# Performance work log

Measured on AMD Instinct MI355X. Metric: run time of the kernel, lower is better.

## Reference

```python
import jax, jax.numpy as jnp
import numpy as np

B, R, N, DN, DR, H, Q, NB = 32, 10, 512, 128, 128, 128, 256, 16


def setup_inputs() -> dict:
    key = jax.random.key(0)
    ks = jax.random.split(key, 14)
    inp = {
        'node_features': jax.random.normal(ks[0], (B, N, DN), jnp.float32),
        'relation_features': jax.random.normal(ks[1], (B, R, DR), jnp.float32),
        'adj': jax.random.uniform(ks[2], (B, R, N, N), jnp.float32),
        'obs': jax.random.normal(ks[3], (B, Q, H), jnp.float32),
        'node_mask': jnp.ones((B, N), jnp.float32),
        'obs_mask': jnp.ones((B, Q), jnp.float32),
        # RGCN params (single layer: hidden_dims=[128])
        'Wb': jax.random.normal(ks[4], (NB, (DN + DR) * R), jnp.float32) * 0.02,  # bottleneck (no bias)
        'Ww': jax.random.normal(ks[5], (H, NB), jnp.float32) * 0.1,               # weight (no bias)
        'rgcn_bias': jnp.zeros((), jnp.float32),                                   # scalar bias (filled 0)
        # ContextQueryAttention params
        'w_C': jax.random.normal(ks[6], (H,), jnp.float32) * 0.05,
        'w_Q': jax.random.normal(ks[7], (H,), jnp.float32) * 0.05,
        'w_CQ': jax.random.normal(ks[8], (H,), jnp.float32) * 0.05,
        'cq_bias': jnp.zeros((), jnp.float32),
        # ReprAggregator output linear (shared for both directions)
        'lin_W': jax.random.normal(ks[9], (H, 4 * H), jnp.float32) * 0.02,
        'lin_b': jnp.zeros((H,), jnp.float32),
    }
    return inp


def _masked_softmax(s, mask, axis):
    return jax.nn.softmax(jnp.where(mask > 0, s, -jnp.inf), axis=axis)


def _rgcn(node_features, relation_features, adj, Wb, Ww, rgcn_bias):
    b, n = node_features.shape[0], node_features.shape[1]
    # per-relation concat: (B,R,N,DN+DR)
    nf = jnp.broadcast_to(node_features[:, None], (b, R, n, node_features.shape[-1]))
    rf = jnp.broadcast_to(relation_features[:, :, None, :], (b, R, n, relation_features.shape[-1]))
    cat = jnp.concatenate([nf, rf], axis=-1)
    # per-relation bmm, gathered in relation order along feature dim: (B,N,R*(DN+DR))
    sup = jnp.einsum('brnm,brmd->bnrd', adj, cat)
    sup = sup.reshape(b, n, R * cat.shape[-1])
    h = sup @ Wb.T            # (B,N,NB)
    h = h @ Ww.T              # (B,N,H)
    return jax.nn.sigmoid(h + rgcn_bias)


def _cqattn(ctx, query, ctx_mask, query_mask, w_C, w_Q, w_CQ, cq_bias):
    # trilinear similarity: (B,Lc,Lq)
    res_C = ctx @ w_C                                  # (B,Lc)
    res_Q = query @ w_Q                                # (B,Lq)
    res_CQ = jnp.einsum('bch,bqh->bcq', ctx * w_CQ, query)
    S = res_C[:, :, None] + res_Q[:, None, :] + res_CQ + cq_bias
    s_ctx = _masked_softmax(S, ctx_mask[:, :, None], axis=1)     # softmax over ctx dim
    s_query = _masked_softmax(S, query_mask[:, None, :], axis=2)  # softmax over query dim
    P = jnp.einsum('bcq,bqh->bch', s_query, query)
    Qm = jnp.einsum('bcq,bdq,bdh->bch', s_query, s_ctx, ctx)
    return jnp.concatenate([ctx, P, ctx * P, ctx * Qm], axis=-1)  # (B,Lc,4H)


def reference(node_features, relation_features, adj, obs, node_mask, obs_mask,
              Wb, Ww, rgcn_bias, w_C, w_Q, w_CQ, cq_bias, lin_W, lin_b):
    # GraphEncoder (single RGCN layer)
    node_repr = _rgcn(node_features, relation_features, adj, Wb, Ww, rgcn_bias)
    # ReprAggregator between obs text repr and node repr
    a1 = _cqattn(obs, node_repr, obs_mask, node_mask, w_C, w_Q, w_CQ, cq_bias)
    a2 = _cqattn(node_repr, obs, node_mask, obs_mask, w_C, w_Q, w_CQ, cq_bias)
    h_og = a1 @ lin_W.T + lin_b   # (B,Q,H)
    h_go = a2 @ lin_W.T + lin_b   # (B,N,H)
    return h_og, h_go
```

## Files before the change

### kernel.cpp

```cpp
#include <hip/hip_runtime.h>
#include <hip/hip_bf16.h>
#include <stdint.h>

typedef unsigned short u16;
typedef __attribute__((ext_vector_type(8))) short short8;
typedef __attribute__((ext_vector_type(4))) float f32x4;

#define DEVI static __device__ __forceinline__

constexpr int B = 32, R = 10, N = 512, H = 128, Q = 256, NB = 16;
constexpr int KWB = 2560;

DEVI u16 f2u(float f) { return __builtin_bit_cast(unsigned short, __float2bfloat16(f)); }
DEVI float u2f(u16 u) { union { uint32_t i; float f; } c; c.i = ((uint32_t)u) << 16; return c.f; }

DEVI float wredmax(float v) { for (int o = 32; o; o >>= 1) v = fmaxf(v, __shfl_xor(v, o)); return v; }
DEVI float wredsum(float v) { for (int o = 32; o; o >>= 1) v += __shfl_xor(v, o); return v; }

__global__ __launch_bounds__(256) void k_prep(
    const float* __restrict__ linW, u16* __restrict__ linWb,
    const float* __restrict__ Wb, u16* __restrict__ WbB,
    const float* __restrict__ Ww, u16* __restrict__ WwB,
    const float* __restrict__ rf, float* __restrict__ vv,
    const float* __restrict__ obs, const float* __restrict__ wC,
    const float* __restrict__ wQ, const float* __restrict__ wCQ,
    u16* __restrict__ obsW, float* __restrict__ a_o, float* __restrict__ d_o) {
  int bid = blockIdx.x, t = threadIdx.x;
  if (bid < 64) {
    int i = bid * 256 + t;
    float4 f = ((const float4*)linW)[i];
    ushort4 o;
    o.x = f2u(f.x); o.y = f2u(f.y); o.z = f2u(f.z); o.w = f2u(f.w);
    ((ushort4*)linWb)[i] = o;
  } else if (bid < 144) {
    int rk = (bid - 64) * 2 + (t >> 7);
    int d = t & 127;
    int r = rk / NB, k = rk % NB;
    WbB[(long)rk * 128 + d] = f2u(Wb[(long)k * KWB + r * 256 + d]);
  } else if (bid < 160) {
    int idx = (bid - 144) * 256 + t;
    int h = idx >> 5, kb = idx & 31;
    WwB[idx] = (kb < NB) ? f2u(Ww[h * NB + kb]) : (u16)0;
  } else if (bid < 1440) {
    int w = t >> 6, lane = t & 63;
    int gid = (bid - 160) * 4 + w;
    int b = gid / (R * NB), rk = gid % (R * NB), r = rk / NB, k = rk % NB;
    float s = 0.f;
    for (int dd = 0; dd < 2; ++dd) {
      int d = lane + dd * 64;
      s += rf[((long)b * R + r) * H + d] * Wb[(long)k * KWB + r * 256 + 128 + d];
    }
    s = wredsum(s);
    if (lane == 0) vv[((long)b * R + r) * NB + k] = s;
  } else {
    int row = (bid - 1440) * 2 + (t >> 7);
    int tt = t & 127;
    float x = obs[(long)row * H + tt];
    obsW[(long)row * H + tt] = f2u(x * wCQ[tt]);
    float aa = wredsum(x * wC[tt]);
    float dd2 = wredsum(x * wQ[tt]);
    __shared__ float sa[4], sd[4];
    int wv = t >> 6;
    if ((t & 63) == 0) { sa[wv] = aa; sd[wv] = dd2; }
    __syncthreads();
    if ((t & 127) == 0) {
      int h = t >> 7;
      a_o[row] = sa[h * 2] + sa[h * 2 + 1];
      d_o[row] = sd[h * 2] + sd[h * 2 + 1];
    }
  }
}

template <bool INF32>
__global__ void k_transpose(const void* __restrict__ in, u16* __restrict__ out, int Rr, int Cc) {
  __shared__ u16 tile[32][33];
  int batch = blockIdx.z;
  int c0 = blockIdx.x * 32, r0 = blockIdx.y * 32;
  int tx = threadIdx.x, ty = threadIdx.y;
  for (int i = 0; i < 4; i++) {
    int r = r0 + ty + i * 8, c = c0 + tx;
    if (INF32) tile[ty + i * 8][tx] = f2u(((const float*)in)[((long)batch * Rr + r) * Cc + c]);
    else       tile[ty + i * 8][tx] = ((const u16*)in)[((long)batch * Rr + r) * Cc + c];
  }
  __syncthreads();
  for (int i = 0; i < 4; i++) {
    int c = c0 + ty + i * 8, r = r0 + tx;
    out[((long)batch * Cc + c) * Rr + r] = tile[tx][ty + i * 8];
  }
}

template <bool AF32, bool BF32, int CMODE, bool TRANSC, int BMODE, bool RGRID, int UNROLL>
__global__ __launch_bounds__(64) void gemm_bt(const void* __restrict__ Av, const void* __restrict__ Btv,
                                              void* __restrict__ Cp, float* __restrict__ C2,
                                              const float* __restrict__ bias,
                                              int Mdim, int Ndim, int Kdim,
                                              long sA, long sBt, long sC, long sC2) {
  int batch = blockIdx.y;
  int ab = batch, bb = batch;
  if (RGRID) { ab = batch % R; bb = batch / R; }
  int ntn = Ndim >> 4;
  int mt = blockIdx.x / ntn, nt = blockIdx.x % ntn;
  int lane = threadIdx.x;
  int rw = lane & 15, kq = lane >> 4;
  long aoff = (long)ab * sA + (long)(mt * 16 + rw) * Kdim + kq * 8;
  long boff = (long)bb * sBt + (long)(nt * 16 + rw) * Kdim + kq * 8;
  f32x4 acc = {0.f, 0.f, 0.f, 0.f};
#pragma unroll UNROLL
  for (int k = 0; k < Kdim; k += 32) {
    short8 av, bv;
    if (AF32) {
      const float* ap = (const float*)Av + aoff + k;
      float4 f0 = *(const float4*)(ap);
      float4 f1 = *(const float4*)(ap + 4);
      av[0] = (short)f2u(f0.x); av[1] = (short)f2u(f0.y);
      av[2] = (short)f2u(f0.z); av[3] = (short)f2u(f0.w);
      av[4] = (short)f2u(f1.x); av[5] = (short)f2u(f1.y);
      av[6] = (short)f2u(f1.z); av[7] = (short)f2u(f1.w);
    } else {
      av = *(const short8*)((const u16*)Av + aoff + k);
    }
    if (BF32) {
      const float* bp = (const float*)Btv + boff + k;
      float4 f0 = *(const float4*)(bp);
      float4 f1 = *(const float4*)(bp + 4);
      bv[0] = (short)f2u(f0.x); bv[1] = (short)f2u(f0.y);
      bv[2] = (short)f2u(f0.z); bv[3] = (short)f2u(f0.w);
      bv[4] = (short)f2u(f1.x); bv[5] = (short)f2u(f1.y);
      bv[6] = (short)f2u(f1.z); bv[7] = (short)f2u(f1.w);
    } else {
      bv = *(const short8*)((const u16*)Btv + boff + k);
    }
    acc = __builtin_amdgcn_mfma_f32_16x16x32_bf16(av, bv, acc, 0, 0, 0);
  }
  int gc = nt * 16 + rw;
  float cb = (BMODE == 1) ? bias[gc] : 0.f;
  for (int i = 0; i < 4; i++) {
    int gr = mt * 16 + (kq * 4 + i);
    float val = acc[i] + cb;
    if (BMODE == 2) val += bias[(long)batch * NB + gr];
    if (CMODE == 2) {
      ((float*)Cp)[(long)batch * sC + (long)gr * Ndim + gc] = val;
      C2[(long)batch * sC2 + (long)gc * Mdim + gr] = val;
    } else {
      long idx = TRANSC ? ((long)gc * Mdim + gr) : ((long)gr * Ndim + gc);
      if (CMODE == 1) ((float*)Cp)[(long)batch * sC + idx] = val;
      else            ((u16*)Cp)[(long)batch * sC + idx] = f2u(val);
    }
  }
}

__global__ __launch_bounds__(256) void k_rgcn(
    const float* __restrict__ adj, const u16* __restrict__ tT,
    const u16* __restrict__ WwB, const float* __restrict__ rb,
    const float* __restrict__ wC, const float* __restrict__ wQ,
    u16* __restrict__ nr, float* __restrict__ b_n, float* __restrict__ c_n) {
  int ntile = blockIdx.x, b = blockIdx.y;
  int n0 = ntile * 16;
  int tid = threadIdx.x;
  int w = tid >> 6, lane = tid & 63;
  int rw = lane & 15, kq = lane >> 4;
  __shared__ float hred[4][16][17];
  __shared__ __align__(16) u16 hbf[16][32];
  __shared__ float bpc[4][16][2];
  float rbv = rb[0];

  f32x4 acc = {0.f, 0.f, 0.f, 0.f};
#pragma unroll 4
  for (int j = 0; j < 40; ++j) {
    int kkk = w + 4 * j;
    int r = kkk >> 4, k = (kkk & 15) * 32;
    const float* ap = adj + (((long)(b * R + r) * N) + n0 + rw) * N + k + kq * 8;
    float4 f0 = *(const float4*)ap;
    float4 f1 = *(const float4*)(ap + 4);
    short8 av;
    av[0] = (short)f2u(f0.x); av[1] = (short)f2u(f0.y);
    av[2] = (short)f2u(f0.z); av[3] = (short)f2u(f0.w);
    av[4] = (short)f2u(f1.x); av[5] = (short)f2u(f1.y);
    av[6] = (short)f2u(f1.z); av[7] = (short)f2u(f1.w);
    short8 bv = *(const short8*)(tT + ((long)(b * R + r) * NB + rw) * N + k + kq * 8);
    acc = __builtin_amdgcn_mfma_f32_16x16x32_bf16(av, bv, acc, 0, 0, 0);
  }
  for (int i = 0; i < 4; i++) hred[w][kq * 4 + i][rw] = acc[i];
  __syncthreads();
  {
    int n = tid >> 4, kb = tid & 15;
    float s = hred[0][n][kb] + hred[1][n][kb] + hred[2][n][kb] + hred[3][n][kb];
    hbf[n][kb] = f2u(s);
    hbf[n][kb + 16] = 0;
  }
  __syncthreads();

  float bsum[4] = {0.f, 0.f, 0.f, 0.f}, csum[4] = {0.f, 0.f, 0.f, 0.f};
  for (int half = 0; half < 2; ++half) {
    int nt = w * 2 + half;
    short8 av = *(const short8*)&hbf[rw][kq * 8];
    short8 bv = *(const short8*)(WwB + (long)(nt * 16 + rw) * 32 + kq * 8);
    f32x4 a2 = {0.f, 0.f, 0.f, 0.f};
    a2 = __builtin_amdgcn_mfma_f32_16x16x32_bf16(av, bv, a2, 0, 0, 0);
    int h = nt * 16 + rw;
    float wq = wQ[h], wc = wC[h];
    for (int i = 0; i < 4; i++) {
      float s = 1.f / (1.f + expf(-(a2[i] + rbv)));
      int n = n0 + kq * 4 + i;
      nr[((long)b * N + n) * H + h] = f2u(s);
      bsum[i] += s * wq;
      csum[i] += s * wc;
    }
  }
  for (int i = 0; i < 4; i++) {
    for (int o = 8; o; o >>= 1) { bsum[i] += __shfl_xor(bsum[i], o); csum[i] += __shfl_xor(csum[i], o); }
  }
  if (rw == 0)
    for (int i = 0; i < 4; i++) { bpc[w][kq * 4 + i][0] = bsum[i]; bpc[w][kq * 4 + i][1] = csum[i]; }
  __syncthreads();
  if (tid < 32) {
    int ns = tid & 15, which = tid >> 4;
    float s = bpc[0][ns][which] + bpc[1][ns][which] + bpc[2][ns][which] + bpc[3][ns][which];
    (which ? c_n : b_n)[(long)b * N + n0 + ns] = s;
  }
}

struct GPar {
  const u16* A; const u16* Bt; u16* C;
  int Mdim; int Kdim; long sA, sBt, sC; int tc;
};
__global__ __launch_bounds__(64) void gemm_quad(GPar p0, GPar p1, GPar p2, GPar p3, int Ndim) {
  int z = blockIdx.z;
  GPar p = (z == 0) ? p0 : (z == 1) ? p1 : (z == 2) ? p2 : p3;
  int batch = blockIdx.y;
  int ntn = Ndim >> 4;
  int mt = blockIdx.x / ntn, nt = blockIdx.x % ntn;
  if (mt * 16 >= p.Mdim) return;
  int lane = threadIdx.x;
  int rw = lane & 15, kq = lane >> 4;
  const u16* ap = p.A + (long)batch * p.sA + (long)(mt * 16 + rw) * p.Kdim + kq * 8;
  const u16* bp = p.Bt + (long)batch * p.sBt + (long)(nt * 16 + rw) * p.Kdim + kq * 8;
  f32x4 acc = {0.f, 0.f, 0.f, 0.f};
#pragma unroll 2
  for (int k = 0; k < p.Kdim; k += 32) {
    short8 av = *(const short8*)(ap + k);
    short8 bv = *(const short8*)(bp + k);
    acc = __builtin_amdgcn_mfma_f32_16x16x32_bf16(av, bv, acc, 0, 0, 0);
  }
  int gc = nt * 16 + rw;
  for (int i = 0; i < 4; i++) {
    int gr = mt * 16 + (kq * 4 + i);
    long idx = p.tc ? ((long)gc * p.Mdim + gr) : ((long)gr * Ndim + gc);
    p.C[(long)batch * p.sC + idx] = f2u(acc[i]);
  }
}

template <bool XF32>
__global__ __launch_bounds__(64) void gemm_cat(const void* __restrict__ Xv, const u16* __restrict__ P,
                                               const u16* __restrict__ Qm, const u16* __restrict__ Wt,
                                               const float* __restrict__ bias, float* __restrict__ out,
                                               int Mdim) {
  int batch = blockIdx.y;
  int ntn = H >> 4;
  int mt = blockIdx.x / ntn, nt = blockIdx.x % ntn;
  int lane = threadIdx.x;
  int rw = lane & 15, kq = lane >> 4;
  long arow = (long)batch * Mdim + (mt * 16 + rw);
  const u16* bp = Wt + (long)(nt * 16 + rw) * (4 * H) + kq * 8;
  f32x4 acc = {0.f, 0.f, 0.f, 0.f};
  for (int k = 0; k < 4 * H; k += 32) {
    int sec = k >> 7;
    int off = (k & 127) + kq * 8;
    long rb2 = arow * H + off;
    short8 av;
    if (sec == 0) {
      if (XF32) {
        const float* xp = (const float*)Xv + rb2;
        float4 f0 = *(const float4*)(xp);
        float4 f1 = *(const float4*)(xp + 4);
        av[0] = (short)f2u(f0.x); av[1] = (short)f2u(f0.y);
        av[2] = (short)f2u(f0.z); av[3] = (short)f2u(f0.w);
        av[4] = (short)f2u(f1.x); av[5] = (short)f2u(f1.y);
        av[6] = (short)f2u(f1.z); av[7] = (short)f2u(f1.w);
      } else {
        av = *(const short8*)((const u16*)Xv + rb2);
      }
    } else if (sec == 1) {
      av = *(const short8*)(P + rb2);
    } else {
      float xf[8];
      if (XF32) {
        const float* xp = (const float*)Xv + rb2;
        float4 f0 = *(const float4*)(xp);
        float4 f1 = *(const float4*)(xp + 4);
        xf[0] = f0.x; xf[1] = f0.y; xf[2] = f0.z; xf[3] = f0.w;
        xf[4] = f1.x; xf[5] = f1.y; xf[6] = f1.z; xf[7] = f1.w;
      } else {
        short8 xv = *(const short8*)((const u16*)Xv + rb2);
        for (int i = 0; i < 8; i++) xf[i] = u2f((u16)xv[i]);
      }
      short8 pv = *(const short8*)((sec == 2 ? P : Qm) + rb2);
      for (int i = 0; i < 8; i++) av[i] = (short)f2u(xf[i] * u2f((u16)pv[i]));
    }
    short8 bv = *(const short8*)(bp + k);
    acc = __builtin_amdgcn_mfma_f32_16x16x32_bf16(av, bv, acc, 0, 0, 0);
  }
  int gc = nt * 16 + rw;
  float cb = bias[gc];
  for (int i = 0; i < 4; i++) {
    int gr = mt * 16 + (kq * 4 + i);
    out[((long)batch * Mdim + gr) * H + gc] = acc[i] + cb;
  }
}

__global__ __launch_bounds__(256) void k_soft_both(
    const float* __restrict__ Mm, const float* __restrict__ MmT,
    const float* __restrict__ b_n, const float* __restrict__ c_n,
    const float* __restrict__ a_o, const float* __restrict__ d_o,
    const float* __restrict__ nmask, const float* __restrict__ omask,
    u16* __restrict__ sq1, u16* __restrict__ sc2,
    u16* __restrict__ sc1T, u16* __restrict__ sq2) {
  int bid = blockIdx.x;
  __shared__ float s1a[4], s2a[4];
  if (bid < B * Q) {
    int b = bid / Q;
    int t = threadIdx.x;
    long ro = bid;
    float v1[2], v2[2];
    for (int i = 0; i < 2; i++) {
      int n = t + 256 * i;
      float mv = Mm[ro * N + n];
      bool on = nmask[(long)b * N + n] > 0.f;
      v1[i] = on ? b_n[(long)b * N + n] + mv : -1e30f;
      v2[i] = on ? c_n[(long)b * N + n] + mv : -1e30f;
    }
    float m1 = wredmax(fmaxf(v1[0], v1[1]));
    float m2 = wredmax(fmaxf(v2[0], v2[1]));
    int wv = t >> 6;
    if ((t & 63) == 0) { s1a[wv] = m1; s2a[wv] = m2; }
    __syncthreads();
    m1 = fmaxf(fmaxf(s1a[0], s1a[1]), fmaxf(s1a[2], s1a[3]));
    m2 = fmaxf(fmaxf(s2a[0], s2a[1]), fmaxf(s2a[2], s2a[3]));
    __syncthreads();
    float e1[2], e2[2];
    e1[0] = expf(v1[0] - m1); e1[1] = expf(v1[1] - m1);
    e2[0] = expf(v2[0] - m2); e2[1] = expf(v2[1] - m2);
    float s1 = wredsum(e1[0] + e1[1]);
    float s2 = wredsum(e2[0] + e2[1]);
    if ((t & 63) == 0) { s1a[wv] = s1; s2a[wv] = s2; }
    __syncthreads();
    float r1 = 1.f / (s1a[0] + s1a[1] + s1a[2] + s1a[3]);
    float r2 = 1.f / (s2a[0] + s2a[1] + s2a[2] + s2a[3]);
    for (int i = 0; i < 2; i++) {
      int n = t + 256 * i;
      sq1[ro * N + n] = f2u(e1[i] * r1);
      sc2[ro * N + n] = f2u(e2[i] * r2);
    }
  } else {
    int id = bid - B * Q;
    int b = id / N;
    int o = threadIdx.x;
    long rn = id;
    float mv = MmT[rn * Q + o];
    bool on = omask[(long)b * Q + o] > 0.f;
    float v1 = on ? a_o[(long)b * Q + o] + mv : -1e30f;
    float v2 = on ? d_o[(long)b * Q + o] + mv : -1e30f;
    float m1 = wredmax(v1), m2 = wredmax(v2);
    int wv = o >> 6;
    if ((o & 63) == 0) { s1a[wv] = m1; s2a[wv] = m2; }
    __syncthreads();
    m1 = fmaxf(fmaxf(s1a[0], s1a[1]), fmaxf(s1a[2], s1a[3]));
    m2 = fmaxf(fmaxf(s2a[0], s2a[1]), fmaxf(s2a[2], s2a[3]));
    __syncthreads();
    float e1 = expf(v1 - m1), e2 = expf(v2 - m2);
    float s1 = wredsum(e1), s2 = wredsum(e2);
    if ((o & 63) == 0) { s1a[wv] = s1; s2a[wv] = s2; }
    __syncthreads();
    float r1 = 1.f / (s1a[0] + s1a[1] + s1a[2] + s1a[3]);
    float r2 = 1.f / (s2a[0] + s2a[1] + s2a[2] + s2a[3]);
    sc1T[rn * Q + o] = f2u(e1 * r1);
    sq2[rn * Q + o] = f2u(e2 * r2);
  }
}

extern "C" void kernel_launch(void* const* d_in, const int* in_sizes, int n_in,
                              void* d_out, int out_size, void* d_ws, size_t ws_size,
                              hipStream_t stream) {
  const float* nf    = (const float*)d_in[0];
  const float* rf    = (const float*)d_in[1];
  const float* adj   = (const float*)d_in[2];
  const float* obs   = (const float*)d_in[3];
  const float* nmask = (const float*)d_in[4];
  const float* omask = (const float*)d_in[5];
  const float* Wb    = (const float*)d_in[6];
  const float* Ww    = (const float*)d_in[7];
  const float* rb    = (const float*)d_in[8];
  const float* wC    = (const float*)d_in[9];
  const float* wQ    = (const float*)d_in[10];
  const float* wCQ   = (const float*)d_in[11];
  const float* linW  = (const float*)d_in[13];
  const float* linb  = (const float*)d_in[14];
  float* outp = (float*)d_out;

  char* w = (char*)d_ws;
  auto alloc = [&](size_t bytes) { char* p = w; w += (bytes + 255) & ~(size_t)255; return p; };
  u16*   linWb = (u16*)  alloc((size_t)H * 4 * H * 2);
  u16*   WbB   = (u16*)  alloc((size_t)R * NB * 128 * 2);
  u16*   WwB   = (u16*)  alloc((size_t)H * 32 * 2);
  float* vv    = (float*)alloc((size_t)B * R * NB * 4);
  u16*   obsW  = (u16*)  alloc((size_t)B * Q * H * 2);
  u16*   obsT  = (u16*)  alloc((size_t)B * H * Q * 2);
  float* a_o   = (float*)alloc((size_t)B * Q * 4);
  float* d_o   = (float*)alloc((size_t)B * Q * 4);
  float* b_n   = (float*)alloc((size_t)B * N * 4);
  float* c_n   = (float*)alloc((size_t)B * N * 4);
  u16*   nr    = (u16*)  alloc((size_t)B * N * H * 2);
  u16*   nrT   = (u16*)  alloc((size_t)B * H * N * 2);
  u16*   tT    = (u16*)  alloc((size_t)B * R * NB * N * 2);
  float* Mm    = (float*)alloc((size_t)B * Q * N * 4);
  float* MmT   = (float*)alloc((size_t)B * N * Q * 4);
  u16*   sq1   = (u16*)  alloc((size_t)B * Q * N * 2);
  u16*   sc2   = (u16*)  alloc((size_t)B * Q * N * 2);
  u16*   sc1T  = (u16*)  alloc((size_t)B * N * Q * 2);
  u16*   sq2   = (u16*)  alloc((size_t)B * N * Q * 2);
  u16*   P1    = (u16*)  alloc((size_t)B * Q * H * 2);
  u16*   T1T   = (u16*)  alloc((size_t)B * H * N * 2);
  u16*   Qm1   = (u16*)  alloc((size_t)B * Q * H * 2);
  u16*   P2    = (u16*)  alloc((size_t)B * N * H * 2);
  u16*   T2T   = (u16*)  alloc((size_t)B * H * Q * 2);
  u16*   Qm2   = (u16*)  alloc((size_t)B * N * H * 2);

  k_prep<<<1440 + B * Q / 2, 256, 0, stream>>>(linW, linWb, Wb, WbB, Ww, WwB,
                                               rf, vv, obs, wC, wQ, wCQ, obsW, a_o, d_o);
  k_transpose<true><<<dim3(H / 32, Q / 32, B), dim3(32, 8), 0, stream>>>(obs, obsT, Q, H);

  gemm_bt<false, true, 0, false, 2, true, 2><<<dim3(N / 16, B * R), 64, 0, stream>>>(
      WbB, nf, tT, nullptr, vv, NB, N, H, (long)NB * 128, (long)N * H, (long)NB * N, 0);
  k_rgcn<<<dim3(N / 16, B), 256, 0, stream>>>(adj, tT, WwB, rb, wC, wQ, nr, b_n, c_n);
  k_transpose<false><<<dim3(H / 32, N / 32, B), dim3(32, 8), 0, stream>>>(nr, nrT, N, H);

  gemm_bt<false, false, 2, false, 0, false, 2><<<dim3((Q / 16) * (N / 16), B), 64, 0, stream>>>(
      obsW, nr, Mm, MmT, nullptr, Q, N, H, (long)Q * H, (long)N * H, (long)Q * N, (long)N * Q);

  k_soft_both<<<B * Q + B * N, 256, 0, stream>>>(Mm, MmT, b_n, c_n, a_o, d_o, nmask, omask,
                                                 sq1, sc2, sc1T, sq2);

  GPar pP1  = {sq1,  nrT,  P1,  Q, N, (long)Q * N, (long)H * N, (long)Q * H, 0};
  GPar pT2T = {sc2,  nrT,  T2T, Q, N, (long)Q * N, (long)H * N, (long)H * Q, 1};
  GPar pT1T = {sc1T, obsT, T1T, N, Q, (long)N * Q, (long)H * Q, (long)H * N, 1};
  GPar pP2  = {sq2,  obsT, P2,  N, Q, (long)N * Q, (long)H * Q, (long)N * H, 0};
  gemm_quad<<<dim3((N / 16) * (H / 16), B, 4), 64, 0, stream>>>(pP1, pT2T, pT1T, pP2, H);
  GPar pQm1 = {sq1, T1T, Qm1, Q, N, (long)Q * N, (long)H * N, (long)Q * H, 0};
  GPar pQm2 = {sq2, T2T, Qm2, N, Q, (long)N * Q, (long)H * Q, (long)N * H, 0};
  gemm_quad<<<dim3((N / 16) * (H / 16), B, 2), 64, 0, stream>>>(pQm1, pQm2, pQm1, pQm2, H);

  gemm_cat<true ><<<dim3((Q / 16) * (H / 16), B), 64, 0, stream>>>(
      obs, P1, Qm1, linWb, linb, outp, Q);
  gemm_cat<false><<<dim3((N / 16) * (H / 16), B), 64, 0, stream>>>(
      nr, P2, Qm2, linWb, linb, outp + (long)B * Q * H, N);

  (void)in_sizes; (void)n_in; (void)out_size; (void)ws_size;
}
```

Measured before the change: 331.9 us.

## Fold transposes into producers, widen GEMM tiles, store scores as bf16

```diff
diff --git a/kernel.cpp b/kernel.cpp
--- a/kernel.cpp
+++ b/kernel.cpp
@@ -16,6 +16,17 @@
 
 DEVI float wredmax(float v) { for (int o = 32; o; o >>= 1) v = fmaxf(v, __shfl_xor(v, o)); return v; }
 DEVI float wredsum(float v) { for (int o = 32; o; o >>= 1) v += __shfl_xor(v, o); return v; }
+
+DEVI short8 cvt8(const float* p) {
+  float4 f0 = *(const float4*)p;
+  float4 f1 = *(const float4*)(p + 4);
+  short8 v;
+  v[0] = (short)f2u(f0.x); v[1] = (short)f2u(f0.y);
+  v[2] = (short)f2u(f0.z); v[3] = (short)f2u(f0.w);
+  v[4] = (short)f2u(f1.x); v[5] = (short)f2u(f1.y);
+  v[6] = (short)f2u(f1.z); v[7] = (short)f2u(f1.w);
+  return v;
+}
 
 __global__ __launch_bounds__(256) void k_prep(
     const float* __restrict__ linW, u16* __restrict__ linWb,
@@ -24,8 +35,11 @@
     const float* __restrict__ rf, float* __restrict__ vv,
     const float* __restrict__ obs, const float* __restrict__ wC,
     const float* __restrict__ wQ, const float* __restrict__ wCQ,
-    u16* __restrict__ obsW, float* __restrict__ a_o, float* __restrict__ d_o) {
+    u16* __restrict__ obsW, float* __restrict__ a_o, float* __restrict__ d_o,
+    u16* __restrict__ obsT) {
   int bid = blockIdx.x, t = threadIdx.x;
+  __shared__ float sa[4], sd[4];
+  __shared__ u16 tile[32][33];
   if (bid < 64) {
     int i = bid * 256 + t;
     float4 f = ((const float4*)linW)[i];
@@ -52,14 +66,13 @@
     }
     s = wredsum(s);
     if (lane == 0) vv[((long)b * R + r) * NB + k] = s;
-  } else {
+  } else if (bid < 5536) {
     int row = (bid - 1440) * 2 + (t >> 7);
     int tt = t & 127;
     float x = obs[(long)row * H + tt];
     obsW[(long)row * H + tt] = f2u(x * wCQ[tt]);
     float aa = wredsum(x * wC[tt]);
     float dd2 = wredsum(x * wQ[tt]);
-    __shared__ float sa[4], sd[4];
     int wv = t >> 6;
     if ((t & 63) == 0) { sa[wv] = aa; sd[wv] = dd2; }
     __syncthreads();
@@ -68,24 +81,20 @@
       a_o[row] = sa[h * 2] + sa[h * 2 + 1];
       d_o[row] = sd[h * 2] + sd[h * 2 + 1];
     }
-  }
-}
-
-template <bool INF32>
-__global__ void k_transpose(const void* __restrict__ in, u16* __restrict__ out, int Rr, int Cc) {
-  __shared__ u16 tile[32][33];
-  int batch = blockIdx.z;
-  int c0 = blockIdx.x * 32, r0 = blockIdx.y * 32;
-  int tx = threadIdx.x, ty = threadIdx.y;
-  for (int i = 0; i < 4; i++) {
-    int r = r0 + ty + i * 8, c = c0 + tx;
-    if (INF32) tile[ty + i * 8][tx] = f2u(((const float*)in)[((long)batch * Rr + r) * Cc + c]);
-    else       tile[ty + i * 8][tx] = ((const u16*)in)[((long)batch * Rr + r) * Cc + c];
-  }
-  __syncthreads();
-  for (int i = 0; i < 4; i++) {
-    int c = c0 + ty + i * 8, r = r0 + tx;
-    out[((long)batch * Cc + c) * Rr + r] = tile[tx][ty + i * 8];
+  } else {
+    int id = bid - 5536;
+    int cx = id & 3, ry = (id >> 2) & 7, b = id >> 5;
+    int c0 = cx * 32, r0 = ry * 32;
+    int tx = t & 31, ty = t >> 5;
+    for (int i = 0; i < 4; i++) {
+      int r = r0 + ty + i * 8, c = c0 + tx;
+      tile[ty + i * 8][tx] = f2u(obs[((long)b * Q + r) * H + c]);
+    }
+    __syncthreads();
+    for (int i = 0; i < 4; i++) {
+      int c = c0 + ty + i * 8, r = r0 + tx;
+      obsT[((long)b * H + c) * Q + r] = tile[tx][ty + i * 8];
+    }
   }
 }
 
@@ -108,28 +117,10 @@
 #pragma unroll UNROLL
   for (int k = 0; k < Kdim; k += 32) {
     short8 av, bv;
-    if (AF32) {
-      const float* ap = (const float*)Av + aoff + k;
-      float4 f0 = *(const float4*)(ap);
-      float4 f1 = *(const float4*)(ap + 4);
-      av[0] = (short)f2u(f0.x); av[1] = (short)f2u(f0.y);
-      av[2] = (short)f2u(f0.z); av[3] = (short)f2u(f0.w);
-      av[4] = (short)f2u(f1.x); av[5] = (short)f2u(f1.y);
-      av[6] = (short)f2u(f1.z); av[7] = (short)f2u(f1.w);
-    } else {
-      av = *(const short8*)((const u16*)Av + aoff + k);
-    }
-    if (BF32) {
-      const float* bp = (const float*)Btv + boff + k;
-      float4 f0 = *(const float4*)(bp);
-      float4 f1 = *(const float4*)(bp + 4);
-      bv[0] = (short)f2u(f0.x); bv[1] = (short)f2u(f0.y);
-      bv[2] = (short)f2u(f0.z); bv[3] = (short)f2u(f0.w);
-      bv[4] = (short)f2u(f1.x); bv[5] = (short)f2u(f1.y);
-      bv[6] = (short)f2u(f1.z); bv[7] = (short)f2u(f1.w);
-    } else {
-      bv = *(const short8*)((const u16*)Btv + boff + k);
-    }
+    if (AF32) av = cvt8((const float*)Av + aoff + k);
+    else      av = *(const short8*)((const u16*)Av + aoff + k);
+    if (BF32) bv = cvt8((const float*)Btv + boff + k);
+    else      bv = *(const short8*)((const u16*)Btv + boff + k);
     acc = __builtin_amdgcn_mfma_f32_16x16x32_bf16(av, bv, acc, 0, 0, 0);
   }
   int gc = nt * 16 + rw;
@@ -153,7 +144,8 @@
     const float* __restrict__ adj, const u16* __restrict__ tT,
     const u16* __restrict__ WwB, const float* __restrict__ rb,
     const float* __restrict__ wC, const float* __restrict__ wQ,
-    u16* __restrict__ nr, float* __restrict__ b_n, float* __restrict__ c_n) {
+    u16* __restrict__ nr, u16* __restrict__ nrT,
+    float* __restrict__ b_n, float* __restrict__ c_n) {
   int ntile = blockIdx.x, b = blockIdx.y;
   int n0 = ntile * 16;
   int tid = threadIdx.x;
@@ -169,14 +161,7 @@
   for (int j = 0; j < 40; ++j) {
     int kkk = w + 4 * j;
     int r = kkk >> 4, k = (kkk & 15) * 32;
-    const float* ap = adj + (((long)(b * R + r) * N) + n0 + rw) * N + k + kq * 8;
-    float4 f0 = *(const float4*)ap;
-    float4 f1 = *(const float4*)(ap + 4);
-    short8 av;
-    av[0] = (short)f2u(f0.x); av[1] = (short)f2u(f0.y);
-    av[2] = (short)f2u(f0.z); av[3] = (short)f2u(f0.w);
-    av[4] = (short)f2u(f1.x); av[5] = (short)f2u(f1.y);
-    av[6] = (short)f2u(f1.z); av[7] = (short)f2u(f1.w);
+    short8 av = cvt8(adj + (((long)(b * R + r) * N) + n0 + rw) * N + k + kq * 8);
     short8 bv = *(const short8*)(tT + ((long)(b * R + r) * NB + rw) * N + k + kq * 8);
     acc = __builtin_amdgcn_mfma_f32_16x16x32_bf16(av, bv, acc, 0, 0, 0);
   }
@@ -202,7 +187,9 @@
     for (int i = 0; i < 4; i++) {
       float s = 1.f / (1.f + expf(-(a2[i] + rbv)));
       int n = n0 + kq * 4 + i;
-      nr[((long)b * N + n) * H + h] = f2u(s);
+      u16 sv = f2u(s);
+      nr[((long)b * N + n) * H + h] = sv;
+      nrT[((long)b * H + h) * N + n] = sv;
       bsum[i] += s * wq;
       csum[i] += s * wc;
     }
@@ -220,96 +207,38 @@
   }
 }
 
-struct GPar {
-  const u16* A; const u16* Bt; u16* C;
-  int Mdim; int Kdim; long sA, sBt, sC; int tc;
-};
-__global__ __launch_bounds__(64) void gemm_quad(GPar p0, GPar p1, GPar p2, GPar p3, int Ndim) {
-  int z = blockIdx.z;
-  GPar p = (z == 0) ? p0 : (z == 1) ? p1 : (z == 2) ? p2 : p3;
-  int batch = blockIdx.y;
-  int ntn = Ndim >> 4;
-  int mt = blockIdx.x / ntn, nt = blockIdx.x % ntn;
-  if (mt * 16 >= p.Mdim) return;
+__global__ __launch_bounds__(64) void k_mm(const u16* __restrict__ obsW, const u16* __restrict__ nr,
+                                           u16* __restrict__ S, u16* __restrict__ ST) {
+  int bx = blockIdx.x;
+  int mt = bx >> 2, ng = bx & 3;
+  int b = blockIdx.y;
   int lane = threadIdx.x;
   int rw = lane & 15, kq = lane >> 4;
-  const u16* ap = p.A + (long)batch * p.sA + (long)(mt * 16 + rw) * p.Kdim + kq * 8;
-  const u16* bp = p.Bt + (long)batch * p.sBt + (long)(nt * 16 + rw) * p.Kdim + kq * 8;
-  f32x4 acc = {0.f, 0.f, 0.f, 0.f};
-#pragma unroll 2
-  for (int k = 0; k < p.Kdim; k += 32) {
+  const u16* ap = obsW + ((long)b * Q + mt * 16 + rw) * H + kq * 8;
+  const u16* bp = nr + ((long)b * N + ng * 128 + rw) * H + kq * 8;
+  f32x4 acc[8] = {};
+  for (int k = 0; k < H; k += 32) {
     short8 av = *(const short8*)(ap + k);
-    short8 bv = *(const short8*)(bp + k);
-    acc = __builtin_amdgcn_mfma_f32_16x16x32_bf16(av, bv, acc, 0, 0, 0);
-  }
-  int gc = nt * 16 + rw;
-  for (int i = 0; i < 4; i++) {
-    int gr = mt * 16 + (kq * 4 + i);
-    long idx = p.tc ? ((long)gc * p.Mdim + gr) : ((long)gr * Ndim + gc);
-    p.C[(long)batch * p.sC + idx] = f2u(acc[i]);
-  }
-}
-
-template <bool XF32>
-__global__ __launch_bounds__(64) void gemm_cat(const void* __restrict__ Xv, const u16* __restrict__ P,
-                                               const u16* __restrict__ Qm, const u16* __restrict__ Wt,
-                                               const float* __restrict__ bias, float* __restrict__ out,
-                                               int Mdim) {
-  int batch = blockIdx.y;
-  int ntn = H >> 4;
-  int mt = blockIdx.x / ntn, nt = blockIdx.x % ntn;
-  int lane = threadIdx.x;
-  int rw = lane & 15, kq = lane >> 4;
-  long arow = (long)batch * Mdim + (mt * 16 + rw);
-  const u16* bp = Wt + (long)(nt * 16 + rw) * (4 * H) + kq * 8;
-  f32x4 acc = {0.f, 0.f, 0.f, 0.f};
-  for (int k = 0; k < 4 * H; k += 32) {
-    int sec = k >> 7;
-    int off = (k & 127) + kq * 8;
-    long rb2 = arow * H + off;
-    short8 av;
-    if (sec == 0) {
-      if (XF32) {
-        const float* xp = (const float*)Xv + rb2;
-        float4 f0 = *(const float4*)(xp);
-        float4 f1 = *(const float4*)(xp + 4);
-        av[0] = (short)f2u(f0.x); av[1] = (short)f2u(f0.y);
-        av[2] = (short)f2u(f0.z); av[3] = (short)f2u(f0.w);
-        av[4] = (short)f2u(f1.x); av[5] = (short)f2u(f1.y);
-        av[6] = (short)f2u(f1.z); av[7] = (short)f2u(f1.w);
-      } else {
-        av = *(const short8*)((const u16*)Xv + rb2);
-      }
-    } else if (sec == 1) {
-      av = *(const short8*)(P + rb2);
-    } else {
-      float xf[8];
-      if (XF32) {
-        const float* xp = (const float*)Xv + rb2;
-        float4 f0 = *(const float4*)(xp);
-        float4 f1 = *(const float4*)(xp + 4);
-        xf[0] = f0.x; xf[1] = f0.y; xf[2] = f0.z; xf[3] = f0.w;
-        xf[4] = f1.x; xf[5] = f1.y; xf[6] = f1.z; xf[7] = f1.w;
-      } else {
-        short8 xv = *(const short8*)((const u16*)Xv + rb2);
-        for (int i = 0; i < 8; i++) xf[i] = u2f((u16)xv[i]);
-      }
-      short8 pv = *(const short8*)((sec == 2 ? P : Qm) + rb2);
-      for (int i = 0; i < 8; i++) av[i] = (short)f2u(xf[i] * u2f((u16)pv[i]));
-    }
-    short8 bv = *(const short8*)(bp + k);
-    acc = __builtin_amdgcn_mfma_f32_16x16x32_bf16(av, bv, acc, 0, 0, 0);
-  }
-  int gc = nt * 16 + rw;
-  float cb = bias[gc];
-  for (int i = 0; i < 4; i++) {
-    int gr = mt * 16 + (kq * 4 + i);
-    out[((long)batch * Mdim + gr) * H + gc] = acc[i] + cb;
+#pragma unroll
+    for (int nt = 0; nt < 8; nt++) {
+      short8 bv = *(const short8*)(bp + (long)nt * 16 * H + k);
+      acc[nt] = __builtin_amdgcn_mfma_f32_16x16x32_bf16(av, bv, acc[nt], 0, 0, 0);
+    }
+  }
+#pragma unroll
+  for (int nt = 0; nt < 8; nt++) {
+    int gc = ng * 128 + nt * 16 + rw;
+    for (int i = 0; i < 4; i++) {
+      int gr = mt * 16 + kq * 4 + i;
+      u16 v = f2u(acc[nt][i]);
+      S[((long)b * Q + gr) * N + gc] = v;
+      ST[((long)b * N + gc) * Q + gr] = v;
+    }
   }
 }
 
 __global__ __launch_bounds__(256) void k_soft_both(
-    const float* __restrict__ Mm, const float* __restrict__ MmT,
+    const u16* __restrict__ S, const u16* __restrict__ ST,
     const float* __restrict__ b_n, const float* __restrict__ c_n,
     const float* __restrict__ a_o, const float* __restrict__ d_o,
     const float* __restrict__ nmask, const float* __restrict__ omask,
@@ -324,7 +253,7 @@
     float v1[2], v2[2];
     for (int i = 0; i < 2; i++) {
       int n = t + 256 * i;
-      float mv = Mm[ro * N + n];
+      float mv = u2f(S[ro * N + n]);
       bool on = nmask[(long)b * N + n] > 0.f;
       v1[i] = on ? b_n[(long)b * N + n] + mv : -1e30f;
       v2[i] = on ? c_n[(long)b * N + n] + mv : -1e30f;
@@ -356,7 +285,7 @@
     int b = id / N;
     int o = threadIdx.x;
     long rn = id;
-    float mv = MmT[rn * Q + o];
+    float mv = u2f(ST[rn * Q + o]);
     bool on = omask[(long)b * Q + o] > 0.f;
     float v1 = on ? a_o[(long)b * Q + o] + mv : -1e30f;
     float v2 = on ? d_o[(long)b * Q + o] + mv : -1e30f;
@@ -375,6 +304,101 @@
     float r2 = 1.f / (s2a[0] + s2a[1] + s2a[2] + s2a[3]);
     sc1T[rn * Q + o] = f2u(e1 * r1);
     sq2[rn * Q + o] = f2u(e2 * r2);
+  }
+}
+
+struct GPar {
+  const u16* A; const u16* Bt; u16* C;
+  int Mdim; int Kdim; long sA, sBt, sC; int tc;
+};
+__global__ __launch_bounds__(64) void gemm_quad8(GPar p0, GPar p1, GPar p2, GPar p3) {
+  int z = blockIdx.z;
+  GPar p = (z == 0) ? p0 : (z == 1) ? p1 : (z == 2) ? p2 : p3;
+  int mt = blockIdx.x;
+  if (mt * 16 >= p.Mdim) return;
+  int batch = blockIdx.y;
+  int lane = threadIdx.x;
+  int rw = lane & 15, kq = lane >> 4;
+  const u16* ap = p.A + (long)batch * p.sA + (long)(mt * 16 + rw) * p.Kdim + kq * 8;
+  const u16* bp = p.Bt + (long)batch * p.sBt + (long)rw * p.Kdim + kq * 8;
+  f32x4 acc[8] = {};
+  for (int k = 0; k < p.Kdim; k += 32) {
+    short8 av = *(const short8*)(ap + k);
+#pragma unroll
+    for (int nt = 0; nt < 8; nt++) {
+      short8 bv = *(const short8*)(bp + (long)nt * 16 * p.Kdim + k);
+      acc[nt] = __builtin_amdgcn_mfma_f32_16x16x32_bf16(av, bv, acc[nt], 0, 0, 0);
+    }
+  }
+#pragma unroll
+  for (int nt = 0; nt < 8; nt++) {
+    int gc = nt * 16 + rw;
+    for (int i = 0; i < 4; i++) {
+      int gr = mt * 16 + kq * 4 + i;
+      long idx = p.tc ? ((long)gc * p.Mdim + gr) : ((long)gr * H + gc);
+      p.C[(long)batch * p.sC + idx] = f2u(acc[nt][i]);
+    }
+  }
+}
+
+__global__ __launch_bounds__(64) void gemm_cat2(
+    const float* __restrict__ obs, const u16* __restrict__ nrr,
+    const u16* __restrict__ P1, const u16* __restrict__ Qm1,
+    const u16* __restrict__ P2, const u16* __restrict__ Qm2,
+    const u16* __restrict__ Wt, const float* __restrict__ bias,
+    float* __restrict__ out0, float* __restrict__ out1) {
+  int z = blockIdx.z;
+  int Mdim = z ? N : Q;
+  int mt = blockIdx.x;
+  if (mt * 16 >= Mdim) return;
+  int batch = blockIdx.y;
+  const u16* P = z ? P2 : P1;
+  const u16* Qm = z ? Qm2 : Qm1;
+  float* out = z ? out1 : out0;
+  int lane = threadIdx.x;
+  int rw = lane & 15, kq = lane >> 4;
+  long arow = (long)batch * Mdim + mt * 16 + rw;
+  const u16* bp = Wt + (long)rw * (4 * H) + kq * 8;
+  f32x4 acc[8] = {};
+  for (int k = 0; k < 4 * H; k += 32) {
+    int sec = k >> 7;
+    int off = (k & 127) + kq * 8;
+    long rb2 = arow * H + off;
+    short8 av;
+    if (sec == 0) {
+      if (!z) av = cvt8(obs + rb2);
+      else    av = *(const short8*)(nrr + rb2);
+    } else if (sec == 1) {
+      av = *(const short8*)(P + rb2);
+    } else {
+      float xf[8];
+      if (!z) {
+        const float* xp = obs + rb2;
+        float4 f0 = *(const float4*)xp;
+        float4 f1 = *(const float4*)(xp + 4);
+        xf[0] = f0.x; xf[1] = f0.y; xf[2] = f0.z; xf[3] = f0.w;
+        xf[4] = f1.x; xf[5] = f1.y; xf[6] = f1.z; xf[7] = f1.w;
+      } else {
+        short8 xv = *(const short8*)(nrr + rb2);
+        for (int i = 0; i < 8; i++) xf[i] = u2f((u16)xv[i]);
+      }
+      short8 pv = *(const short8*)((sec == 2 ? P : Qm) + rb2);
+      for (int i = 0; i < 8; i++) av[i] = (short)f2u(xf[i] * u2f((u16)pv[i]));
+    }
+#pragma unroll
+    for (int nt = 0; nt < 8; nt++) {
+      short8 bv = *(const short8*)(bp + (long)nt * 16 * (4 * H) + k);
+      acc[nt] = __builtin_amdgcn_mfma_f32_16x16x32_bf16(av, bv, acc[nt], 0, 0, 0);
+    }
+  }
+#pragma unroll
+  for (int nt = 0; nt < 8; nt++) {
+    int gc = nt * 16 + rw;
+    float cb = bias[gc];
+    for (int i = 0; i < 4; i++) {
+      int gr = mt * 16 + kq * 4 + i;
+      out[((long)batch * Mdim + gr) * H + gc] = acc[nt][i] + cb;
+    }
   }
 }
 
@@ -412,8 +436,8 @@
   u16*   nr    = (u16*)  alloc((size_t)B * N * H * 2);
   u16*   nrT   = (u16*)  alloc((size_t)B * H * N * 2);
   u16*   tT    = (u16*)  alloc((size_t)B * R * NB * N * 2);
-  float* Mm    = (float*)alloc((size_t)B * Q * N * 4);
-  float* MmT   = (float*)alloc((size_t)B * N * Q * 4);
+  u16*   S     = (u16*)  alloc((size_t)B * Q * N * 2);
+  u16*   ST    = (u16*)  alloc((size_t)B * N * Q * 2);
   u16*   sq1   = (u16*)  alloc((size_t)B * Q * N * 2);
   u16*   sc2   = (u16*)  alloc((size_t)B * Q * N * 2);
   u16*   sc1T  = (u16*)  alloc((size_t)B * N * Q * 2);
@@ -425,34 +449,24 @@
   u16*   T2T   = (u16*)  alloc((size_t)B * H * Q * 2);
   u16*   Qm2   = (u16*)  alloc((size_t)B * N * H * 2);
 
-  k_prep<<<1440 + B * Q / 2, 256, 0, stream>>>(linW, linWb, Wb, WbB, Ww, WwB,
-                                               rf, vv, obs, wC, wQ, wCQ, obsW, a_o, d_o);
-  k_transpose<true><<<dim3(H / 32, Q / 32, B), dim3(32, 8), 0, stream>>>(obs, obsT, Q, H);
-
+  k_prep<<<6560, 256, 0, stream>>>(linW, linWb, Wb, WbB, Ww, WwB,
+                                   rf, vv, obs, wC, wQ, wCQ, obsW, a_o, d_o, obsT);
   gemm_bt<false, true, 0, false, 2, true, 2><<<dim3(N / 16, B * R), 64, 0, stream>>>(
       WbB, nf, tT, nullptr, vv, NB, N, H, (long)NB * 128, (long)N * H, (long)NB * N, 0);
-  k_rgcn<<<dim3(N / 16, B), 256, 0, stream>>>(adj, tT, WwB, rb, wC, wQ, nr, b_n, c_n);
-  k_transpose<false><<<dim3(H / 32, N / 32, B), dim3(32, 8), 0, stream>>>(nr, nrT, N, H);
-
-  gemm_bt<false, false, 2, false, 0, false, 2><<<dim3((Q / 16) * (N / 16), B), 64, 0, stream>>>(
-      obsW, nr, Mm, MmT, nullptr, Q, N, H, (long)Q * H, (long)N * H, (long)Q * N, (long)N * Q);
-
-  k_soft_both<<<B * Q + B * N, 256, 0, stream>>>(Mm, MmT, b_n, c_n, a_o, d_o, nmask, omask,
+  k_rgcn<<<dim3(N / 16, B), 256, 0, stream>>>(adj, tT, WwB, rb, wC, wQ, nr, nrT, b_n, c_n);
+  k_mm<<<dim3((Q / 16) * (N / 128), B), 64, 0, stream>>>(obsW, nr, S, ST);
+  k_soft_both<<<B * Q + B * N, 256, 0, stream>>>(S, ST, b_n, c_n, a_o, d_o, nmask, omask,
                                                  sq1, sc2, sc1T, sq2);
-
   GPar pP1  = {sq1,  nrT,  P1,  Q, N, (long)Q * N, (long)H * N, (long)Q * H, 0};
   GPar pT2T = {sc2,  nrT,  T2T, Q, N, (long)Q * N, (long)H * N, (long)H * Q, 1};
   GPar pT1T = {sc1T, obsT, T1T, N, Q, (long)N * Q, (long)H * Q, (long)H * N, 1};
   GPar pP2  = {sq2,  obsT, P2,  N, Q, (long)N * Q, (long)H * Q, (long)N * H, 0};
-  gemm_quad<<<dim3((N / 16) * (H / 16), B, 4), 64, 0, stream>>>(pP1, pT2T, pT1T, pP2, H);
+  gemm_quad8<<<dim3(N / 16, B, 4), 64, 0, stream>>>(pP1, pT2T, pT1T, pP2);
   GPar pQm1 = {sq1, T1T, Qm1, Q, N, (long)Q * N, (long)H * N, (long)Q * H, 0};
   GPar pQm2 = {sq2, T2T, Qm2, N, Q, (long)N * Q, (long)H * Q, (long)N * H, 0};
-  gemm_quad<<<dim3((N / 16) * (H / 16), B, 2), 64, 0, stream>>>(pQm1, pQm2, pQm1, pQm2, H);
-
-  gemm_cat<true ><<<dim3((Q / 16) * (H / 16), B), 64, 0, stream>>>(
-      obs, P1, Qm1, linWb, linb, outp, Q);
-  gemm_cat<false><<<dim3((N / 16) * (H / 16), B), 64, 0, stream>>>(
-      nr, P2, Qm2, linWb, linb, outp + (long)B * Q * H, N);
+  gemm_quad8<<<dim3(N / 16, B, 2), 64, 0, stream>>>(pQm1, pQm2, pQm1, pQm2);
+  gemm_cat2<<<dim3(N / 16, B, 2), 64, 0, stream>>>(obs, nr, P1, Qm1, P2, Qm2,
+                                                   linWb, linb, outp, outp + (long)B * Q * H);
 
   (void)in_sizes; (void)n_in; (void)out_size; (void)ws_size;
 }
```

After: 297.6 us. -10.4%, faster.
